# Performance work log

Measured on AMD Instinct MI355X. Metric: run time of the kernel, lower is better.

The kernel has to match this reference:

```python
import jax, jax.numpy as jnp
import numpy as np

T, B, E, H = 2048, 2, 1024, 16

def setup_inputs() -> dict:
    rng = jax.random.key(0)
    ks = jax.random.split(rng, 7)
    s = 0.02
    return {
        "query": jax.random.normal(ks[0], (T, B, E), jnp.float32),
        "key": jax.random.normal(ks[1], (T, B, E), jnp.float32),
        "value": jax.random.normal(ks[2], (T, B, E), jnp.float32),
        "in_proj_weight": jax.random.normal(ks[3], (3 * E, E), jnp.float32) * s,
        "in_proj_bias": jax.random.normal(ks[4], (3 * E,), jnp.float32) * s,
        "out_proj_weight": jax.random.normal(ks[5], (E, E), jnp.float32) * s,
        "out_proj_bias": jax.random.normal(ks[6], (E,), jnp.float32) * s,
    }

def reference(query, key, value, in_proj_weight, in_proj_bias, out_proj_weight, out_proj_bias):
    tgt_len, bsz, embed_dim = query.shape
    num_heads = H
    head_dim = embed_dim // num_heads
    scaling = head_dim ** -0.5
    wq, wk, wv = jnp.split(in_proj_weight, 3, axis=0)
    bq, bk, bv = jnp.split(in_proj_bias, 3, axis=0)
    # projections: F.linear(x, W, b) = x @ W.T + b
    q = (query @ wq.T + bq) * scaling          # (T, B, E)
    k = key @ wk.T + bk                        # (S, B, E)
    v = value @ wv.T + bv                      # (S, B, E)
    # (len, B, E) -> (B*H, len, head_dim), matching torch view+transpose
    def to_heads(x):
        L = x.shape[0]
        return x.reshape(L, bsz * num_heads, head_dim).transpose(1, 0, 2)
    q, k, v = to_heads(q), to_heads(k), to_heads(v)
    scores = jnp.einsum('bqd,bkd->bqk', q, k)  # (B*H, T, S)
    attn = jax.nn.softmax(scores, axis=-1)
    out = jnp.einsum('bqk,bkd->bqd', attn, v)  # (B*H, T, head_dim)
    out = out.transpose(1, 0, 2).reshape(tgt_len, bsz, embed_dim)
    out = out @ out_proj_weight.T + out_proj_bias
    return out
```

## Files before the change

### kernel.cpp

```cpp
#include <hip/hip_runtime.h>
#include <cstdint>
#include <cstddef>

#define QSCALE 0.18033688011112042f

typedef __attribute__((ext_vector_type(8))) short bf16x8;
typedef __attribute__((ext_vector_type(4))) float f32x4;

#define MFMA(a, b, c) __builtin_amdgcn_mfma_f32_16x16x32_bf16(a, b, c, 0, 0, 0)

typedef union { unsigned int u[4]; bf16x8 b; } pku;

__device__ __forceinline__ unsigned short cvt_bf16(float x) {
  union { float f; unsigned int u; } v;
  v.f = x;
  unsigned int r = v.u + 0x7FFFu + ((v.u >> 16) & 1u);
  return (unsigned short)(r >> 16);
}

__device__ __forceinline__ void gll16(const void* g, void* l) {
  __builtin_amdgcn_global_load_lds(
      (const __attribute__((address_space(1))) unsigned int*)g,
      (__attribute__((address_space(3))) unsigned int*)l, 16, 0, 0);
}

__device__ __forceinline__ float fast_exp2(float x) {
#if __has_builtin(__builtin_amdgcn_exp2f)
  return __builtin_amdgcn_exp2f(x);
#else
  float r; asm("v_exp_f32 %0, %1" : "=v"(r) : "v"(x)); return r;
#endif
}

__device__ __forceinline__ unsigned int pack_bf16(float lo, float hi) {
  union { float f; unsigned int u; } a, b;
  a.f = lo; b.f = hi;
  return __builtin_amdgcn_perm(b.u + 0x8000u, a.u + 0x8000u, 0x07060302u);
}

__global__ void cvt_all(const float* __restrict__ q,
                        const float* __restrict__ k,
                        const float* __restrict__ v,
                        const float* __restrict__ ipw,
                        const float* __restrict__ opw,
                        unsigned short* __restrict__ dst) {
  const size_t i = ((size_t)blockIdx.x * 256 + threadIdx.x) * 8;
  const float* src;
  float scale = 1.0f;
  if (i < 4194304) src = q + i;
  else if (i < 8388608) src = k + (i - 4194304);
  else if (i < 12582912) src = v + (i - 8388608);
  else {
    const size_t w = i - 12582912;
    if (w < 3145728) { src = ipw + w; if (w < 1048576) scale = QSCALE; }
    else src = opw + (w - 3145728);
  }
  float4 a = *(const float4*)src;
  float4 b = *(const float4*)(src + 4);
  uint4 o;
  o.x = cvt_bf16(a.x * scale) | ((unsigned int)cvt_bf16(a.y * scale) << 16);
  o.y = cvt_bf16(a.z * scale) | ((unsigned int)cvt_bf16(a.w * scale) << 16);
  o.z = cvt_bf16(b.x * scale) | ((unsigned int)cvt_bf16(b.y * scale) << 16);
  o.w = cvt_bf16(b.z * scale) | ((unsigned int)cvt_bf16(b.w * scale) << 16);
  *(uint4*)(dst + i) = o;
}

__global__ __launch_bounds__(256, 3) void gemm_qkv(
    const unsigned short* __restrict__ X,
    const unsigned short* __restrict__ W,
    const float* __restrict__ bias,
    unsigned short* __restrict__ Qh,
    unsigned short* __restrict__ Kh,
    unsigned short* __restrict__ Vt)
{
  __shared__ unsigned short As[128 * 64];
  __shared__ unsigned short Bs[128 * 64];
  const int tid = threadIdx.x;
  const int wave = tid >> 6, lane = tid & 63;
  const int quad = lane >> 4, l16 = lane & 15;
  const int flat = blockIdx.x + (blockIdx.y << 3) + (blockIdx.z << 8);
  const int nf = (flat & 7) * 96 + (flat >> 3);
  const int z = nf >> 8;
  const int m0 = ((nf >> 3) & 31) * 128;
  const int n0 = (nf & 7) * 128;
  const unsigned short* Ab = X + (size_t)z * 4194304 + (size_t)m0 * 1024;
  const unsigned short* Bb = W + ((size_t)z * 1024 + n0) * 1024;
  const int wr = (wave >> 1) * 64, wc = (wave & 1) * 64;

  const f32x4 z4 = {0.f, 0.f, 0.f, 0.f};
  f32x4 acc[4][4];
#pragma unroll
  for (int i = 0; i < 4; ++i)
#pragma unroll
    for (int j = 0; j < 4; ++j) acc[i][j] = z4;

  for (int k0 = 0; k0 < 1024; k0 += 64) {
    __syncthreads();
#pragma unroll
    for (int j = 0; j < 4; ++j) {
      const int c = j * 256 + tid;
      const int row = c >> 3, pc = c & 7;
      const int kc = pc ^ (row & 7);
      gll16(Ab + (size_t)row * 1024 + k0 + kc * 8, &As[c * 8]);
      gll16(Bb + (size_t)row * 1024 + k0 + kc * 8, &Bs[c * 8]);
    }
    __syncthreads();
#pragma unroll
    for (int kk = 0; kk < 2; ++kk) {
      bf16x8 af[4], bfr[4];
#pragma unroll
      for (int rt = 0; rt < 4; ++rt) {
        const int row = wr + rt * 16 + l16;
        af[rt] = *(const bf16x8*)&As[row * 64 + ((kk * 4 + quad) ^ (row & 7)) * 8];
      }
#pragma unroll
      for (int ct = 0; ct < 4; ++ct) {
        const int row = wc + ct * 16 + l16;
        bfr[ct] = *(const bf16x8*)&Bs[row * 64 + ((kk * 4 + quad) ^ (row & 7)) * 8];
      }
#pragma unroll
      for (int rt = 0; rt < 4; ++rt)
#pragma unroll
        for (int ct = 0; ct < 4; ++ct)
          acc[rt][ct] = MFMA(af[rt], bfr[ct], acc[rt][ct]);
    }
  }

#pragma unroll
  for (int rt = 0; rt < 4; ++rt)
#pragma unroll
    for (int ct = 0; ct < 4; ++ct) {
      const int gn = n0 + wc + ct * 16 + l16;
      float bv = bias[z * 1024 + gn];
      if (z == 0) bv *= QSCALE;
      const int h = gn >> 6, d = gn & 63;
#pragma unroll
      for (int r = 0; r < 4; ++r) {
        const int gm = m0 + wr + rt * 16 + quad * 4 + r;
        const int t = gm >> 1, b = gm & 1;
        const int bh = b * 16 + h;
        const unsigned short o = cvt_bf16(acc[rt][ct][r] + bv);
        if (z == 0)      Qh[((size_t)bh * 2048 + t) * 64 + d] = o;
        else if (z == 1) Kh[((size_t)bh * 2048 + t) * 64 + d] = o;
        else {
          const int w32 = t & 31;
          const int tp = (t & ~31) | (((w32 >> 2) & 3) << 3) | ((w32 >> 4) << 2) | (w32 & 3);
          Vt[((size_t)bh * 64 + d) * 2048 + tp] = o;
        }
      }
    }
}

__global__ __launch_bounds__(256, 2) void attn(
    const unsigned short* __restrict__ Qh,
    const unsigned short* __restrict__ Kh,
    const unsigned short* __restrict__ Vt,
    unsigned short* __restrict__ O)
{
  __shared__ unsigned short KV[16384];
  __shared__ float Ls[128];
  unsigned short* Ks = KV;
  unsigned short* Vs = KV + 8192;
  const int tid = threadIdx.x;
  const int wave = tid >> 6, lane = tid & 63;
  const int quad = lane >> 4, l16 = lane & 15;
  const int pair = wave >> 1, kh = wave & 1;
  const int flat = blockIdx.x + (blockIdx.y << 4);
  const int nf = (flat & 7) * 64 + (flat >> 3);
  const int qt = nf & 15, bh = nf >> 4;
  const unsigned short* Qb = Qh + ((size_t)bh * 2048 + qt * 128 + pair * 64) * 64;
  const unsigned short* Kb = Kh + (size_t)bh * 2048 * 64;
  const unsigned short* Vb = Vt + (size_t)bh * 64 * 2048;

  bf16x8 qf[4][2];
#pragma unroll
  for (int g = 0; g < 4; ++g)
#pragma unroll
    for (int kk = 0; kk < 2; ++kk)
      qf[g][kk] = *(const bf16x8*)(Qb + (size_t)(g * 16 + l16) * 64 + kk * 32 + quad * 8);

  const unsigned short* kp[4];
  const unsigned short* vp[4];
  unsigned short* kl[4];
  unsigned short* vl[4];
#pragma unroll
  for (int j = 0; j < 4; ++j) {
    const int c = wave * 256 + j * 64 + lane;
    const int r = c >> 3, cc = c & 7;
    kp[j] = Kb + (size_t)r * 64 + (cc ^ (r & 7)) * 8;
    kl[j] = &Ks[c * 8];
    const int r2 = c >> 4, cc2 = c & 15;
    vp[j] = Vb + (size_t)r2 * 2048 + (cc2 ^ (r2 & 15)) * 8;
    vl[j] = &Vs[c * 8];
  }

  pku ones;
  ones.u[0] = ones.u[1] = ones.u[2] = ones.u[3] = 0x3F803F80u;

  const f32x4 z4 = {0.f, 0.f, 0.f, 0.f};
  f32x4 oacc[4][4];
  f32x4 lacc[4] = {z4, z4, z4, z4};
#pragma unroll
  for (int g = 0; g < 4; ++g)
#pragma unroll
    for (int c = 0; c < 4; ++c) oacc[g][c] = z4;

#pragma unroll 1
  for (int it = 0; it < 16; ++it) {
    __syncthreads();
#pragma unroll
    for (int j = 0; j < 4; ++j) {
      gll16(kp[j], kl[j]);
      gll16(vp[j], vl[j]);
      kp[j] += 128 * 64;
      vp[j] += 128;
    }
    __syncthreads();

#pragma unroll
    for (int jj = 0; jj < 2; ++jj) {
      unsigned int pk0[4][2], pk1[4][2];
#pragma unroll
      for (int half = 0; half < 2; ++half) {
        const int ct = jj * 2 + half;
        const int R = kh * 64 + ct * 16 + l16;
        bf16x8 kfr[2];
#pragma unroll
        for (int kk = 0; kk < 2; ++kk)
          kfr[kk] = *(const bf16x8*)&Ks[R * 64 + ((kk * 4 + quad) ^ (R & 7)) * 8];
#pragma unroll
        for (int g = 0; g < 4; ++g) {
          f32x4 sv = z4;
          sv = MFMA(kfr[0], qf[g][0], sv);
          sv = MFMA(kfr[1], qf[g][1], sv);
          f32x4 p;
#pragma unroll
          for (int r = 0; r < 4; ++r) p[r] = fast_exp2(sv[r]);
          pk0[g][half] = pack_bf16(p[0], p[1]);
          pk1[g][half] = pack_bf16(p[2], p[3]);
        }
      }
      const int jjg = kh * 2 + jj;
#pragma unroll
      for (int ctd = 0; ctd < 4; ++ctd) {
        const int R = ctd * 16 + l16;
        const int phys = (jjg * 4 + quad) ^ (R & 15);
        const bf16x8 vv = *(const bf16x8*)&Vs[R * 128 + phys * 8];
#pragma unroll
        for (int g = 0; g < 4; ++g) {
          pku a;
          a.u[0] = pk0[g][0]; a.u[1] = pk1[g][0];
          a.u[2] = pk0[g][1]; a.u[3] = pk1[g][1];
          oacc[g][ctd] = MFMA(a.b, vv, oacc[g][ctd]);
        }
      }
#pragma unroll
      for (int g = 0; g < 4; ++g) {
        pku a;
        a.u[0] = pk0[g][0]; a.u[1] = pk1[g][0];
        a.u[2] = pk0[g][1]; a.u[3] = pk1[g][1];
        lacc[g] = MFMA(a.b, ones.b, lacc[g]);
      }
    }
  }

  __syncthreads();
  float* Fp = (float*)KV;
  if (kh == 1) {
#pragma unroll
    for (int g = 0; g < 4; ++g) {
#pragma unroll
      for (int ctd = 0; ctd < 4; ++ctd)
#pragma unroll
        for (int r = 0; r < 4; ++r)
          Fp[pair * 4096 + (g * 16 + quad * 4 + r) * 64 + ctd * 16 + l16] = oacc[g][ctd][r];
#pragma unroll
      for (int r = 0; r < 4; ++r)
        Ls[pair * 64 + g * 16 + quad * 4 + r] = lacc[g][r];
    }
  }
  __syncthreads();
  if (kh == 0) {
    const int b = bh >> 4, h = bh & 15;
#pragma unroll
    for (int g = 0; g < 4; ++g)
#pragma unroll
      for (int r = 0; r < 4; ++r) {
        const int ql = g * 16 + quad * 4 + r;
        const float lv = lacc[g][r] + Ls[pair * 64 + ql];
        const float inv = 1.0f / lv;
        const int t = qt * 128 + pair * 64 + ql;
#pragma unroll
        for (int ctd = 0; ctd < 4; ++ctd) {
          const float val = oacc[g][ctd][r] + Fp[pair * 4096 + ql * 64 + ctd * 16 + l16];
          O[((size_t)t * 2 + b) * 1024 + h * 64 + ctd * 16 + l16] = cvt_bf16(val * inv);
        }
      }
  }
}

__global__ __launch_bounds__(256, 4) void gemm_out(
    const unsigned short* __restrict__ A,
    const unsigned short* __restrict__ W,
    const float* __restrict__ bias,
    float* __restrict__ out)
{
  __shared__ unsigned short As[128 * 64];
  __shared__ unsigned short Bs[64 * 64];
  const int tid = threadIdx.x;
  const int wave = tid >> 6, lane = tid & 63;
  const int quad = lane >> 4, l16 = lane & 15;
  const int flat = blockIdx.x + (blockIdx.y << 4);
  const int nf = (flat & 7) * 64 + (flat >> 3);
  const int m0 = (nf >> 4) * 128;
  const int n0 = (nf & 15) * 64;
  const unsigned short* Ab = A + (size_t)m0 * 1024;
  const unsigned short* Bb = W + (size_t)n0 * 1024;
  const int wr = (wave >> 1) * 64, wc = (wave & 1) * 32;

  const f32x4 z4 = {0.f, 0.f, 0.f, 0.f};
  f32x4 acc[4][2];
#pragma unroll
  for (int i = 0; i < 4; ++i)
#pragma unroll
    for (int j = 0; j < 2; ++j) acc[i][j] = z4;

  for (int k0 = 0; k0 < 1024; k0 += 64) {
    __syncthreads();
#pragma unroll
    for (int j = 0; j < 4; ++j) {
      const int c = j * 256 + tid;
      const int row = c >> 3, pc = c & 7;
      const int kc = pc ^ (row & 7);
      gll16(Ab + (size_t)row * 1024 + k0 + kc * 8, &As[c * 8]);
    }
#pragma unroll
    for (int j = 0; j < 2; ++j) {
      const int c = j * 256 + tid;
      const int row = c >> 3, pc = c & 7;
      const int kc = pc ^ (row & 7);
      gll16(Bb + (size_t)row * 1024 + k0 + kc * 8, &Bs[c * 8]);
    }
    __syncthreads();
#pragma unroll
    for (int kk = 0; kk < 2; ++kk) {
      bf16x8 af[4], bfr[2];
#pragma unroll
      for (int rt = 0; rt < 4; ++rt) {
        const int row = wr + rt * 16 + l16;
        af[rt] = *(const bf16x8*)&As[row * 64 + ((kk * 4 + quad) ^ (row & 7)) * 8];
      }
#pragma unroll
      for (int ct = 0; ct < 2; ++ct) {
        const int row = wc + ct * 16 + l16;
        bfr[ct] = *(const bf16x8*)&Bs[row * 64 + ((kk * 4 + quad) ^ (row & 7)) * 8];
      }
#pragma unroll
      for (int rt = 0; rt < 4; ++rt)
#pragma unroll
        for (int ct = 0; ct < 2; ++ct)
          acc[rt][ct] = MFMA(af[rt], bfr[ct], acc[rt][ct]);
    }
  }

#pragma unroll
  for (int rt = 0; rt < 4; ++rt)
#pragma unroll
    for (int ct = 0; ct < 2; ++ct) {
      const int gn = n0 + wc + ct * 16 + l16;
      const float bv = bias[gn];
#pragma unroll
      for (int r = 0; r < 4; ++r) {
        const int gm = m0 + wr + rt * 16 + quad * 4 + r;
        out[(size_t)gm * 1024 + gn] = acc[rt][ct][r] + bv;
      }
    }
}

extern "C" void kernel_launch(void* const* d_in, const int* in_sizes, int n_in,
                              void* d_out, int out_size, void* d_ws, size_t ws_size,
                              hipStream_t stream) {
  const float* q   = (const float*)d_in[0];
  const float* k   = (const float*)d_in[1];
  const float* v   = (const float*)d_in[2];
  const float* ipw = (const float*)d_in[3];
  const float* ipb = (const float*)d_in[4];
  const float* opw = (const float*)d_in[5];
  const float* opb = (const float*)d_in[6];

  unsigned short* ws = (unsigned short*)d_ws;
  unsigned short* X  = ws;
  unsigned short* Wb = ws + 12582912;
  unsigned short* Wo = ws + 15728640;
  unsigned short* Qh = ws + 16777216;
  unsigned short* Kh = ws + 20971520;
  unsigned short* Vx = ws + 25165824;
  unsigned short* Oa = ws + 29360128;

  cvt_all<<<dim3(8192), 256, 0, stream>>>(q, k, v, ipw, opw, ws);
  gemm_qkv<<<dim3(8, 32, 3), 256, 0, stream>>>(X, Wb, ipb, Qh, Kh, Vx);
  attn<<<dim3(16, 32), 256, 0, stream>>>(Qh, Kh, Vx, Oa);
  gemm_out<<<dim3(16, 32), 256, 0, stream>>>(Oa, Wo, opb, (float*)d_out);
}
```

Measured before the change: 210.5 us.

## Double-buffer LDS tiles in attention and output GEMM to overlap loads

Both the attention kernel and the output projection GEMM now use two LDS buffers. The next K/V or A/B tile is prefetched with global_load_lds while the current tile is consumed, so only one barrier per iteration remains. This doubles shared memory use, and the GEMM's launch bounds drop from 4 to 2 blocks per CU, which may reduce occupancy. One barrier per iteration is only enough if the hardware waits for the async LDS loads to finish at that barrier.

```diff
diff --git a/kernel.cpp b/kernel.cpp
--- a/kernel.cpp
+++ b/kernel.cpp
@@ -157,10 +157,8 @@
     const unsigned short* __restrict__ Vt,
     unsigned short* __restrict__ O)
 {
-  __shared__ unsigned short KV[16384];
+  __shared__ unsigned short KV[2][16384];
   __shared__ float Ls[128];
-  unsigned short* Ks = KV;
-  unsigned short* Vs = KV + 8192;
   const int tid = threadIdx.x;
   const int wave = tid >> 6, lane = tid & 63;
   const int quad = lane >> 4, l16 = lane & 15;
@@ -181,17 +179,16 @@
 
   const unsigned short* kp[4];
   const unsigned short* vp[4];
-  unsigned short* kl[4];
-  unsigned short* vl[4];
+  int klo[4], vlo[4];
 #pragma unroll
   for (int j = 0; j < 4; ++j) {
     const int c = wave * 256 + j * 64 + lane;
     const int r = c >> 3, cc = c & 7;
     kp[j] = Kb + (size_t)r * 64 + (cc ^ (r & 7)) * 8;
-    kl[j] = &Ks[c * 8];
+    klo[j] = c * 8;
     const int r2 = c >> 4, cc2 = c & 15;
     vp[j] = Vb + (size_t)r2 * 2048 + (cc2 ^ (r2 & 15)) * 8;
-    vl[j] = &Vs[c * 8];
+    vlo[j] = 8192 + c * 8;
   }
 
   pku ones;
@@ -205,17 +202,29 @@
 #pragma unroll
     for (int c = 0; c < 4; ++c) oacc[g][c] = z4;
 
+#pragma unroll
+  for (int j = 0; j < 4; ++j) {
+    gll16(kp[j], &KV[0][klo[j]]);
+    gll16(vp[j], &KV[0][vlo[j]]);
+    kp[j] += 128 * 64;
+    vp[j] += 128;
+  }
+  __syncthreads();
+
 #pragma unroll 1
   for (int it = 0; it < 16; ++it) {
-    __syncthreads();
-#pragma unroll
-    for (int j = 0; j < 4; ++j) {
-      gll16(kp[j], kl[j]);
-      gll16(vp[j], vl[j]);
-      kp[j] += 128 * 64;
-      vp[j] += 128;
-    }
-    __syncthreads();
+    const int cur = it & 1;
+    if (it < 15) {
+#pragma unroll
+      for (int j = 0; j < 4; ++j) {
+        gll16(kp[j], &KV[cur ^ 1][klo[j]]);
+        gll16(vp[j], &KV[cur ^ 1][vlo[j]]);
+        kp[j] += 128 * 64;
+        vp[j] += 128;
+      }
+    }
+    const unsigned short* Ks = KV[cur];
+    const unsigned short* Vs = KV[cur] + 8192;
 
 #pragma unroll
     for (int jj = 0; jj < 2; ++jj) {
@@ -262,9 +271,9 @@
         lacc[g] = MFMA(a.b, ones.b, lacc[g]);
       }
     }
-  }
-
-  __syncthreads();
+    __syncthreads();
+  }
+
   float* Fp = (float*)KV;
   if (kh == 1) {
 #pragma unroll
@@ -299,14 +308,14 @@
   }
 }
 
-__global__ __launch_bounds__(256, 4) void gemm_out(
+__global__ __launch_bounds__(256, 2) void gemm_out(
     const unsigned short* __restrict__ A,
     const unsigned short* __restrict__ W,
     const float* __restrict__ bias,
     float* __restrict__ out)
 {
-  __shared__ unsigned short As[128 * 64];
-  __shared__ unsigned short Bs[64 * 64];
+  __shared__ unsigned short As[2][128 * 64];
+  __shared__ unsigned short Bs[2][64 * 64];
   const int tid = threadIdx.x;
   const int wave = tid >> 6, lane = tid & 63;
   const int quad = lane >> 4, l16 = lane & 15;
@@ -318,42 +327,48 @@
   const unsigned short* Bb = W + (size_t)n0 * 1024;
   const int wr = (wave >> 1) * 64, wc = (wave & 1) * 32;
 
-  const f32x4 z4 = {0.f, 0.f, 0.f, 0.f};
-  f32x4 acc[4][2];
-#pragma unroll
-  for (int i = 0; i < 4; ++i)
-#pragma unroll
-    for (int j = 0; j < 2; ++j) acc[i][j] = z4;
-
-  for (int k0 = 0; k0 < 1024; k0 += 64) {
-    __syncthreads();
+  auto stage = [&](int k0, int buf) {
 #pragma unroll
     for (int j = 0; j < 4; ++j) {
       const int c = j * 256 + tid;
       const int row = c >> 3, pc = c & 7;
       const int kc = pc ^ (row & 7);
-      gll16(Ab + (size_t)row * 1024 + k0 + kc * 8, &As[c * 8]);
+      gll16(Ab + (size_t)row * 1024 + k0 + kc * 8, &As[buf][c * 8]);
     }
 #pragma unroll
     for (int j = 0; j < 2; ++j) {
       const int c = j * 256 + tid;
       const int row = c >> 3, pc = c & 7;
       const int kc = pc ^ (row & 7);
-      gll16(Bb + (size_t)row * 1024 + k0 + kc * 8, &Bs[c * 8]);
-    }
-    __syncthreads();
+      gll16(Bb + (size_t)row * 1024 + k0 + kc * 8, &Bs[buf][c * 8]);
+    }
+  };
+
+  const f32x4 z4 = {0.f, 0.f, 0.f, 0.f};
+  f32x4 acc[4][2];
+#pragma unroll
+  for (int i = 0; i < 4; ++i)
+#pragma unroll
+    for (int j = 0; j < 2; ++j) acc[i][j] = z4;
+
+  stage(0, 0);
+  __syncthreads();
+
+  for (int k0 = 0; k0 < 1024; k0 += 64) {
+    const int cur = (k0 >> 6) & 1;
+    if (k0 < 960) stage(k0 + 64, cur ^ 1);
 #pragma unroll
     for (int kk = 0; kk < 2; ++kk) {
       bf16x8 af[4], bfr[2];
 #pragma unroll
       for (int rt = 0; rt < 4; ++rt) {
         const int row = wr + rt * 16 + l16;
-        af[rt] = *(const bf16x8*)&As[row * 64 + ((kk * 4 + quad) ^ (row & 7)) * 8];
+        af[rt] = *(const bf16x8*)&As[cur][row * 64 + ((kk * 4 + quad) ^ (row & 7)) * 8];
       }
 #pragma unroll
       for (int ct = 0; ct < 2; ++ct) {
         const int row = wc + ct * 16 + l16;
-        bfr[ct] = *(const bf16x8*)&Bs[row * 64 + ((kk * 4 + quad) ^ (row & 7)) * 8];
+        bfr[ct] = *(const bf16x8*)&Bs[cur][row * 64 + ((kk * 4 + quad) ^ (row & 7)) * 8];
       }
 #pragma unroll
       for (int rt = 0; rt < 4; ++rt)
@@ -361,6 +376,7 @@
         for (int ct = 0; ct < 2; ++ct)
           acc[rt][ct] = MFMA(af[rt], bfr[ct], acc[rt][ct]);
     }
+    __syncthreads();
   }
 
 #pragma unroll
```

Result: no change. 211.2 us (+0.4%).

## Restructure attention so each wave owns 16 query rows over full key tile

Applied to the files above, without the earlier changes.

Attention blocks now cover 64 query rows instead of 128, and each wave handles 16 query rows across all 128 keys per tile. This replaces the earlier split of the key dimension between wave pairs, so the LDS reduction of partial outputs and row sums at the end goes away and the grid doubles to 1024 blocks. Launch bounds go up to 4 blocks per SM, and s_setprio is raised around the PV MFMAs. In exchange, each K/V tile loaded into LDS is reused by half as many query rows, which doubles total K/V global traffic.

```diff
diff --git a/kernel.cpp b/kernel.cpp
--- a/kernel.cpp
+++ b/kernel.cpp
@@ -151,33 +151,29 @@
     }
 }
 
-__global__ __launch_bounds__(256, 2) void attn(
+__global__ __launch_bounds__(256, 4) void attn(
     const unsigned short* __restrict__ Qh,
     const unsigned short* __restrict__ Kh,
     const unsigned short* __restrict__ Vt,
     unsigned short* __restrict__ O)
 {
   __shared__ unsigned short KV[16384];
-  __shared__ float Ls[128];
   unsigned short* Ks = KV;
   unsigned short* Vs = KV + 8192;
   const int tid = threadIdx.x;
   const int wave = tid >> 6, lane = tid & 63;
   const int quad = lane >> 4, l16 = lane & 15;
-  const int pair = wave >> 1, kh = wave & 1;
-  const int flat = blockIdx.x + (blockIdx.y << 4);
-  const int nf = (flat & 7) * 64 + (flat >> 3);
-  const int qt = nf & 15, bh = nf >> 4;
-  const unsigned short* Qb = Qh + ((size_t)bh * 2048 + qt * 128 + pair * 64) * 64;
+  const int flat = blockIdx.x + (blockIdx.y << 5);
+  const int nf = (flat & 7) * 128 + (flat >> 3);
+  const int qt = nf & 31, bh = nf >> 5;
+  const unsigned short* Qb = Qh + ((size_t)bh * 2048 + qt * 64 + wave * 16) * 64;
   const unsigned short* Kb = Kh + (size_t)bh * 2048 * 64;
   const unsigned short* Vb = Vt + (size_t)bh * 64 * 2048;
 
-  bf16x8 qf[4][2];
-#pragma unroll
-  for (int g = 0; g < 4; ++g)
-#pragma unroll
-    for (int kk = 0; kk < 2; ++kk)
-      qf[g][kk] = *(const bf16x8*)(Qb + (size_t)(g * 16 + l16) * 64 + kk * 32 + quad * 8);
+  bf16x8 qf[2];
+#pragma unroll
+  for (int kk = 0; kk < 2; ++kk)
+    qf[kk] = *(const bf16x8*)(Qb + (size_t)l16 * 64 + kk * 32 + quad * 8);
 
   const unsigned short* kp[4];
   const unsigned short* vp[4];
@@ -198,12 +194,10 @@
   ones.u[0] = ones.u[1] = ones.u[2] = ones.u[3] = 0x3F803F80u;
 
   const f32x4 z4 = {0.f, 0.f, 0.f, 0.f};
-  f32x4 oacc[4][4];
-  f32x4 lacc[4] = {z4, z4, z4, z4};
-#pragma unroll
-  for (int g = 0; g < 4; ++g)
-#pragma unroll
-    for (int c = 0; c < 4; ++c) oacc[g][c] = z4;
+  f32x4 oacc[4];
+  f32x4 lacc = z4;
+#pragma unroll
+  for (int c = 0; c < 4; ++c) oacc[c] = z4;
 
 #pragma unroll 1
   for (int it = 0; it < 16; ++it) {
@@ -218,84 +212,50 @@
     __syncthreads();
 
 #pragma unroll
-    for (int jj = 0; jj < 2; ++jj) {
-      unsigned int pk0[4][2], pk1[4][2];
+    for (int jj = 0; jj < 4; ++jj) {
+      unsigned int pk0[2], pk1[2];
 #pragma unroll
       for (int half = 0; half < 2; ++half) {
         const int ct = jj * 2 + half;
-        const int R = kh * 64 + ct * 16 + l16;
+        const int R = ct * 16 + l16;
         bf16x8 kfr[2];
 #pragma unroll
         for (int kk = 0; kk < 2; ++kk)
           kfr[kk] = *(const bf16x8*)&Ks[R * 64 + ((kk * 4 + quad) ^ (R & 7)) * 8];
-#pragma unroll
-        for (int g = 0; g < 4; ++g) {
-          f32x4 sv = z4;
-          sv = MFMA(kfr[0], qf[g][0], sv);
-          sv = MFMA(kfr[1], qf[g][1], sv);
-          f32x4 p;
-#pragma unroll
-          for (int r = 0; r < 4; ++r) p[r] = fast_exp2(sv[r]);
-          pk0[g][half] = pack_bf16(p[0], p[1]);
-          pk1[g][half] = pack_bf16(p[2], p[3]);
-        }
-      }
-      const int jjg = kh * 2 + jj;
+        f32x4 sv = z4;
+        sv = MFMA(kfr[0], qf[0], sv);
+        sv = MFMA(kfr[1], qf[1], sv);
+        f32x4 p;
+#pragma unroll
+        for (int r = 0; r < 4; ++r) p[r] = fast_exp2(sv[r]);
+        pk0[half] = pack_bf16(p[0], p[1]);
+        pk1[half] = pack_bf16(p[2], p[3]);
+      }
+      pku a;
+      a.u[0] = pk0[0]; a.u[1] = pk1[0];
+      a.u[2] = pk0[1]; a.u[3] = pk1[1];
+      __builtin_amdgcn_s_setprio(1);
 #pragma unroll
       for (int ctd = 0; ctd < 4; ++ctd) {
         const int R = ctd * 16 + l16;
-        const int phys = (jjg * 4 + quad) ^ (R & 15);
+        const int phys = (jj * 4 + quad) ^ (R & 15);
         const bf16x8 vv = *(const bf16x8*)&Vs[R * 128 + phys * 8];
-#pragma unroll
-        for (int g = 0; g < 4; ++g) {
-          pku a;
-          a.u[0] = pk0[g][0]; a.u[1] = pk1[g][0];
-          a.u[2] = pk0[g][1]; a.u[3] = pk1[g][1];
-          oacc[g][ctd] = MFMA(a.b, vv, oacc[g][ctd]);
-        }
-      }
-#pragma unroll
-      for (int g = 0; g < 4; ++g) {
-        pku a;
-        a.u[0] = pk0[g][0]; a.u[1] = pk1[g][0];
-        a.u[2] = pk0[g][1]; a.u[3] = pk1[g][1];
-        lacc[g] = MFMA(a.b, ones.b, lacc[g]);
-      }
-    }
-  }
-
-  __syncthreads();
-  float* Fp = (float*)KV;
-  if (kh == 1) {
-#pragma unroll
-    for (int g = 0; g < 4; ++g) {
-#pragma unroll
-      for (int ctd = 0; ctd < 4; ++ctd)
-#pragma unroll
-        for (int r = 0; r < 4; ++r)
-          Fp[pair * 4096 + (g * 16 + quad * 4 + r) * 64 + ctd * 16 + l16] = oacc[g][ctd][r];
-#pragma unroll
-      for (int r = 0; r < 4; ++r)
-        Ls[pair * 64 + g * 16 + quad * 4 + r] = lacc[g][r];
-    }
-  }
-  __syncthreads();
-  if (kh == 0) {
-    const int b = bh >> 4, h = bh & 15;
-#pragma unroll
-    for (int g = 0; g < 4; ++g)
-#pragma unroll
-      for (int r = 0; r < 4; ++r) {
-        const int ql = g * 16 + quad * 4 + r;
-        const float lv = lacc[g][r] + Ls[pair * 64 + ql];
-        const float inv = 1.0f / lv;
-        const int t = qt * 128 + pair * 64 + ql;
-#pragma unroll
-        for (int ctd = 0; ctd < 4; ++ctd) {
-          const float val = oacc[g][ctd][r] + Fp[pair * 4096 + ql * 64 + ctd * 16 + l16];
-          O[((size_t)t * 2 + b) * 1024 + h * 64 + ctd * 16 + l16] = cvt_bf16(val * inv);
-        }
-      }
+        oacc[ctd] = MFMA(a.b, vv, oacc[ctd]);
+      }
+      lacc = MFMA(a.b, ones.b, lacc);
+      __builtin_amdgcn_s_setprio(0);
+    }
+  }
+
+  const int b = bh >> 4, h = bh & 15;
+#pragma unroll
+  for (int r = 0; r < 4; ++r) {
+    const float inv = 1.0f / lacc[r];
+    const int t = qt * 64 + wave * 16 + quad * 4 + r;
+#pragma unroll
+    for (int ctd = 0; ctd < 4; ++ctd)
+      O[((size_t)t * 2 + b) * 1024 + h * 64 + ctd * 16 + l16] =
+          cvt_bf16(oacc[ctd][r] * inv);
   }
 }
 
@@ -399,6 +359,6 @@
 
   cvt_all<<<dim3(8192), 256, 0, stream>>>(q, k, v, ipw, opw, ws);
   gemm_qkv<<<dim3(8, 32, 3), 256, 0, stream>>>(X, Wb, ipb, Qh, Kh, Vx);
-  attn<<<dim3(16, 32), 256, 0, stream>>>(Qh, Kh, Vx, Oa);
+  attn<<<dim3(32, 32), 256, 0, stream>>>(Qh, Kh, Vx, Oa);
   gemm_out<<<dim3(16, 32), 256, 0, stream>>>(Oa, Wo, opb, (float*)d_out);
 }
```

New measurement: 211.9 us. About the same (+0.7%).
